# Kernel tuning notes

Measured on AMD Instinct MI355X. Metric: run time of the kernel, lower is better.

Reference implementation:

```python
import jax, jax.numpy as jnp
import numpy as np

B, N_KERNELS, IN_DIM, UNITS = 512, 128, 1024, 1024

def setup_inputs() -> dict:
    key = jax.random.key(0)
    k1, k2 = jax.random.split(key)
    x = jax.random.normal(k1, (B, N_KERNELS, IN_DIM), dtype=jnp.float32)
    kernels = jax.random.normal(k2, (N_KERNELS, IN_DIM, UNITS), dtype=jnp.float32) * 0.02
    return {"x": x, "kernels": kernels}

def reference(x, kernels):
    # Original loops over n_kernels doing x[:, i:i+1, :] @ kernels[i] then softplus.
    # Note: the original's K.bias_add return value is discarded, so bias never
    # affects the output; the faithful math has no bias term.
    # Batched GEMM over the position axis k: [B,K,I] x [K,I,O] -> [B,K,O]
    out = jax.nn.softplus(jnp.einsum('bki,kio->bko', x, kernels))
    return out
```

## Files before the change

kernel.cpp:

```cpp
#include <hip/hip_runtime.h>

#define NKER  128
#define INDIM 1024
#define UNITS 1024

typedef __attribute__((ext_vector_type(8)))  short          bf16x8;
typedef __attribute__((ext_vector_type(4)))  float          f32x4;
typedef __attribute__((ext_vector_type(4)))  unsigned short u16x4;
typedef __attribute__((ext_vector_type(8)))  unsigned short u16x8;

#define LGKM0   asm volatile("s_waitcnt lgkmcnt(0)" ::: "memory")
#define BAR()   __builtin_amdgcn_s_barrier()
#define SCHED0  __builtin_amdgcn_sched_barrier(0)

__device__ __forceinline__ unsigned short f2bf(float f) {
    return __builtin_bit_cast(unsigned short, static_cast<__bf16>(f));
}

__device__ __forceinline__ int swzidx(int r, int k) {
    return r * 32 + ((((k >> 3) ^ ((r >> 1) & 3)) << 3) | (k & 7));
}

struct Stage {
    f32x4 av[4];
    float bv[8];
};

__global__ void __launch_bounds__(512, 2)
dense_local(const float* __restrict__ X, const float* __restrict__ Kn,
            float* __restrict__ Out)
{
    __shared__ __align__(16) unsigned short lA[2][256 * 32];
    __shared__ __align__(16) unsigned short lB[2][128 * 32];

    const int bid  = blockIdx.x;
    const int wg   = (bid & 7) * 256 + (bid >> 3);
    const int kidx = wg >> 4;
    const int tile = wg & 15;
    const int mt   = tile >> 3;
    const int nt   = tile & 7;

    const int t   = threadIdx.x;
    const int l   = t & 63;
    const int w   = t >> 6;
    const int wm  = w >> 1;
    const int wn  = w & 1;
    const int l15 = l & 15, g = l >> 4;

    const size_t MROW = (size_t)NKER * INDIM;

    const float* Abase = X   + (size_t)mt * 256 * MROW + (size_t)kidx * INDIM;
    const float* Bbase = Kn  + (size_t)kidx * INDIM * UNITS + nt * 128;
    float*       Cbase = Out + (size_t)mt * 256 * MROW + (size_t)kidx * UNITS + nt * 128;

    const int ar0 = t >> 3;
    const int ak4 = (t & 7) << 2;
    const int bn  = t & 127;
    const int bkh = t >> 7;

    const float* aTh = Abase + (size_t)ar0 * MROW + ak4;
    const float* bTh = Bbase + (size_t)bkh * 8 * UNITS + bn;
    const float* aP0 = aTh;                const float* bP0 = bTh;
    const float* aP1 = aTh + 32;           const float* bP1 = bTh + (size_t)32 * UNITS;

    f32x4 acc[4][4];
#pragma unroll
    for (int mi = 0; mi < 4; ++mi)
#pragma unroll
        for (int ni = 0; ni < 4; ++ni)
            acc[mi][ni] = f32x4{0.f, 0.f, 0.f, 0.f};

    Stage S0, S1;

    auto loadg = [&](Stage& S, const float*& aP, const float*& bP) {
#pragma unroll
        for (int p = 0; p < 4; ++p)
            S.av[p] = *(const f32x4*)(aP + (size_t)p * 64 * MROW);
#pragma unroll
        for (int j = 0; j < 8; ++j)
            S.bv[j] = bP[(size_t)j * UNITS];
        aP += 64;
        bP += (size_t)64 * UNITS;
    };

    auto writes = [&](const Stage& S, int bb) {
#pragma unroll
        for (int p = 0; p < 4; ++p) {
            u16x4 h;
#pragma unroll
            for (int c = 0; c < 4; ++c) h[c] = f2bf(S.av[p][c]);
            *(u16x4*)&lA[bb][swzidx(ar0 + p * 64, ak4)] = h;
        }
        u16x8 h0;
#pragma unroll
        for (int j = 0; j < 8; ++j) h0[j] = f2bf(S.bv[j]);
        *(u16x8*)&lB[bb][swzidx(bn, bkh * 8)] = h0;
    };

    auto compute = [&](int bb) {
        bf16x8 af[4], bfr[4];
#pragma unroll
        for (int mi = 0; mi < 4; ++mi)
            af[mi] = *(const bf16x8*)&lA[bb][swzidx(wm * 64 + mi * 16 + l15, g * 8)];
#pragma unroll
        for (int ni = 0; ni < 4; ++ni)
            bfr[ni] = *(const bf16x8*)&lB[bb][swzidx(wn * 64 + ni * 16 + l15, g * 8)];
        LGKM0;
        SCHED0;
        __builtin_amdgcn_s_setprio(1);
#pragma unroll
        for (int mi = 0; mi < 4; ++mi)
#pragma unroll
            for (int ni = 0; ni < 4; ++ni)
                acc[mi][ni] = __builtin_amdgcn_mfma_f32_16x16x32_bf16(
                    af[mi], bfr[ni], acc[mi][ni], 0, 0, 0);
        __builtin_amdgcn_s_setprio(0);
    };

    loadg(S0, aP0, bP0);
    loadg(S1, aP1, bP1);
    writes(S0, 0);
    LGKM0;
    BAR();

#pragma unroll 1
    for (int it = 0; it < 15; ++it) {
        loadg(S0, aP0, bP0);
        compute(0);
        BAR();
        writes(S1, 1);
        LGKM0;
        BAR();
        loadg(S1, aP1, bP1);
        compute(1);
        BAR();
        writes(S0, 0);
        LGKM0;
        BAR();
    }

    compute(0);
    BAR();
    writes(S1, 1);
    LGKM0;
    BAR();
    compute(1);

#pragma unroll
    for (int mi = 0; mi < 4; ++mi) {
#pragma unroll
        for (int ni = 0; ni < 4; ++ni) {
            const int n = wn * 64 + ni * 16 + l15;
#pragma unroll
            for (int r = 0; r < 4; ++r) {
                const int m = wm * 64 + mi * 16 + g * 4 + r;
                const float v  = acc[mi][ni][r];
                const float sp = fmaxf(v, 0.0f) + log1pf(__expf(-fabsf(v)));
                Cbase[(size_t)m * MROW + n] = sp;
            }
        }
    }
}

extern "C" void kernel_launch(void* const* d_in, const int* in_sizes, int n_in,
                              void* d_out, int out_size, void* d_ws, size_t ws_size,
                              hipStream_t stream) {
    const float* X  = (const float*)d_in[0];
    const float* Kn = (const float*)d_in[1];
    float* O = (float*)d_out;
    dense_local<<<2048, 512, 0, stream>>>(X, Kn, O);
}
```

Before: 453.1 us.

## Load A fragments directly into registers, dropping the LDS staging for A

A tile rows are now read from global memory straight into the MFMA operand layout, converted to bf16 in registers, and never pass through shared memory. Waves are re-split so each wave owns 32 rows and all 128 columns (2x8 MFMA tiles), which removes the A shared-memory writes and reads and halves LDS use. In exchange each wave re-reads the full B tile from LDS, and the A global loads become less coalesced: each lane reads 32 bytes with a stride of a full row.

```diff
diff --git a/kernel.cpp b/kernel.cpp
--- a/kernel.cpp
+++ b/kernel.cpp
@@ -6,7 +6,6 @@
 
 typedef __attribute__((ext_vector_type(8)))  short          bf16x8;
 typedef __attribute__((ext_vector_type(4)))  float          f32x4;
-typedef __attribute__((ext_vector_type(4)))  unsigned short u16x4;
 typedef __attribute__((ext_vector_type(8)))  unsigned short u16x8;
 
 #define LGKM0   asm volatile("s_waitcnt lgkmcnt(0)" ::: "memory")
@@ -21,16 +20,10 @@
     return r * 32 + ((((k >> 3) ^ ((r >> 1) & 3)) << 3) | (k & 7));
 }
 
-struct Stage {
-    f32x4 av[4];
-    float bv[8];
-};
-
 __global__ void __launch_bounds__(512, 2)
 dense_local(const float* __restrict__ X, const float* __restrict__ Kn,
             float* __restrict__ Out)
 {
-    __shared__ __align__(16) unsigned short lA[2][256 * 32];
     __shared__ __align__(16) unsigned short lB[2][128 * 32];
 
     const int bid  = blockIdx.x;
@@ -43,8 +36,6 @@
     const int t   = threadIdx.x;
     const int l   = t & 63;
     const int w   = t >> 6;
-    const int wm  = w >> 1;
-    const int wn  = w & 1;
     const int l15 = l & 15, g = l >> 4;
 
     const size_t MROW = (size_t)NKER * INDIM;
@@ -53,107 +44,115 @@
     const float* Bbase = Kn  + (size_t)kidx * INDIM * UNITS + nt * 128;
     float*       Cbase = Out + (size_t)mt * 256 * MROW + (size_t)kidx * UNITS + nt * 128;
 
-    const int ar0 = t >> 3;
-    const int ak4 = (t & 7) << 2;
-    const int bn  = t & 127;
-    const int bkh = t >> 7;
+    const float* aP = Abase + (size_t)(w * 32 + l15) * MROW + g * 8;
+    const int bn = t & 127, bkh = t >> 7;
+    const float* bP0 = Bbase + (size_t)bkh * 8 * UNITS + bn;
+    const float* bP1 = bP0 + (size_t)32 * UNITS;
 
-    const float* aTh = Abase + (size_t)ar0 * MROW + ak4;
-    const float* bTh = Bbase + (size_t)bkh * 8 * UNITS + bn;
-    const float* aP0 = aTh;                const float* bP0 = bTh;
-    const float* aP1 = aTh + 32;           const float* bP1 = bTh + (size_t)32 * UNITS;
-
-    f32x4 acc[4][4];
+    f32x4 acc[2][8];
 #pragma unroll
-    for (int mi = 0; mi < 4; ++mi)
+    for (int mi = 0; mi < 2; ++mi)
 #pragma unroll
-        for (int ni = 0; ni < 4; ++ni)
+        for (int ni = 0; ni < 8; ++ni)
             acc[mi][ni] = f32x4{0.f, 0.f, 0.f, 0.f};
 
-    Stage S0, S1;
+    f32x4 aw[2][2];
+    float s0[8], s1[8];
 
-    auto loadg = [&](Stage& S, const float*& aP, const float*& bP) {
+    auto loadA = [&]() {
 #pragma unroll
-        for (int p = 0; p < 4; ++p)
-            S.av[p] = *(const f32x4*)(aP + (size_t)p * 64 * MROW);
+        for (int mi = 0; mi < 2; ++mi) {
+            const float* p = aP + (size_t)mi * 16 * MROW;
+            aw[mi][0] = *(const f32x4*)(p);
+            aw[mi][1] = *(const f32x4*)(p + 4);
+        }
+        aP += 32;
+    };
+    auto loadB = [&](float* S, const float*& bP) {
 #pragma unroll
         for (int j = 0; j < 8; ++j)
-            S.bv[j] = bP[(size_t)j * UNITS];
-        aP += 64;
+            S[j] = bP[(size_t)j * UNITS];
         bP += (size_t)64 * UNITS;
     };
-
-    auto writes = [&](const Stage& S, int bb) {
+    auto writeB = [&](const float* S, int bb) {
+        u16x8 h;
 #pragma unroll
-        for (int p = 0; p < 4; ++p) {
-            u16x4 h;
-#pragma unroll
-            for (int c = 0; c < 4; ++c) h[c] = f2bf(S.av[p][c]);
-            *(u16x4*)&lA[bb][swzidx(ar0 + p * 64, ak4)] = h;
-        }
-        u16x8 h0;
-#pragma unroll
-        for (int j = 0; j < 8; ++j) h0[j] = f2bf(S.bv[j]);
-        *(u16x8*)&lB[bb][swzidx(bn, bkh * 8)] = h0;
+        for (int j = 0; j < 8; ++j) h[j] = f2bf(S[j]);
+        *(u16x8*)&lB[bb][swzidx(bn, bkh * 8)] = h;
     };
 
-    auto compute = [&](int bb) {
-        bf16x8 af[4], bfr[4];
+    bf16x8 af[2];
+    auto cvtA = [&]() {
 #pragma unroll
-        for (int mi = 0; mi < 4; ++mi)
-            af[mi] = *(const bf16x8*)&lA[bb][swzidx(wm * 64 + mi * 16 + l15, g * 8)];
+        for (int mi = 0; mi < 2; ++mi) {
+            u16x8 h;
 #pragma unroll
-        for (int ni = 0; ni < 4; ++ni)
-            bfr[ni] = *(const bf16x8*)&lB[bb][swzidx(wn * 64 + ni * 16 + l15, g * 8)];
+            for (int c = 0; c < 4; ++c) {
+                h[c]     = f2bf(aw[mi][0][c]);
+                h[c + 4] = f2bf(aw[mi][1][c]);
+            }
+            af[mi] = __builtin_bit_cast(bf16x8, h);
+        }
+    };
+
+    bf16x8 bfr[8];
+    auto readB = [&](int bb) {
+#pragma unroll
+        for (int ni = 0; ni < 8; ++ni)
+            bfr[ni] = *(const bf16x8*)&lB[bb][swzidx(ni * 16 + l15, g * 8)];
+    };
+    auto domfma = [&]() {
         LGKM0;
         SCHED0;
         __builtin_amdgcn_s_setprio(1);
 #pragma unroll
-        for (int mi = 0; mi < 4; ++mi)
+        for (int mi = 0; mi < 2; ++mi)
 #pragma unroll
-            for (int ni = 0; ni < 4; ++ni)
+            for (int ni = 0; ni < 8; ++ni)
                 acc[mi][ni] = __builtin_amdgcn_mfma_f32_16x16x32_bf16(
                     af[mi], bfr[ni], acc[mi][ni], 0, 0, 0);
         __builtin_amdgcn_s_setprio(0);
     };
 
-    loadg(S0, aP0, bP0);
-    loadg(S1, aP1, bP1);
-    writes(S0, 0);
+    loadB(s0, bP0);
+    loadB(s1, bP1);
+    loadA();
+    writeB(s0, 0);
     LGKM0;
     BAR();
 
 #pragma unroll 1
-    for (int it = 0; it < 15; ++it) {
-        loadg(S0, aP0, bP0);
-        compute(0);
+    for (int it = 0; it < 16; ++it) {
+        cvtA();
+        loadA();
+        readB(0);
+        if (it < 15) loadB(s0, bP0);
+        domfma();
         BAR();
-        writes(S1, 1);
+        writeB(s1, 1);
         LGKM0;
         BAR();
-        loadg(S1, aP1, bP1);
-        compute(1);
-        BAR();
-        writes(S0, 0);
-        LGKM0;
-        BAR();
+        cvtA();
+        if (it < 15) loadA();
+        readB(1);
+        if (it < 15) loadB(s1, bP1);
+        domfma();
+        if (it < 15) {
+            BAR();
+            writeB(s0, 0);
+            LGKM0;
+            BAR();
+        }
     }
 
-    compute(0);
-    BAR();
-    writes(S1, 1);
-    LGKM0;
-    BAR();
-    compute(1);
-
 #pragma unroll
-    for (int mi = 0; mi < 4; ++mi) {
+    for (int mi = 0; mi < 2; ++mi) {
 #pragma unroll
-        for (int ni = 0; ni < 4; ++ni) {
-            const int n = wn * 64 + ni * 16 + l15;
+        for (int ni = 0; ni < 8; ++ni) {
+            const int n = ni * 16 + l15;
 #pragma unroll
             for (int r = 0; r < 4; ++r) {
-                const int m = wm * 64 + mi * 16 + g * 4 + r;
+                const int m = w * 32 + mi * 16 + g * 4 + r;
                 const float v  = acc[mi][ni][r];
                 const float sp = fmaxf(v, 0.0f) + log1pf(__expf(-fabsf(v)));
                 Cbase[(size_t)m * MROW + n] = sp;
```

After: 561.7 us. 24.0% more time.

## Restructure K-loop into 64-wide tiles split into two interleaved half-phases

Applied to the files above, without the earlier changes.

Each iteration now covers a 64-wide K chunk held as two 32-wide LDS sub-buffers, double-buffered across iterations. The A and B global loads, bf16 conversion and LDS writes for the next chunk are spread across the two MFMA half-phases of the current chunk. The aim is to overlap global memory latency and LDS writes with matrix compute and to reduce the barrier stalls per K step. In exchange, LDS use doubles, more staging registers are live, and there are four barriers per 64-K step, which may hurt occupancy at 2 blocks per CU.

```diff
diff --git a/kernel.cpp b/kernel.cpp
--- a/kernel.cpp
+++ b/kernel.cpp
@@ -21,17 +21,12 @@
     return r * 32 + ((((k >> 3) ^ ((r >> 1) & 3)) << 3) | (k & 7));
 }
 
-struct Stage {
-    f32x4 av[4];
-    float bv[8];
-};
-
 __global__ void __launch_bounds__(512, 2)
 dense_local(const float* __restrict__ X, const float* __restrict__ Kn,
             float* __restrict__ Out)
 {
-    __shared__ __align__(16) unsigned short lA[2][256 * 32];
-    __shared__ __align__(16) unsigned short lB[2][128 * 32];
+    __shared__ __align__(16) unsigned short lA[2][2][256 * 32];
+    __shared__ __align__(16) unsigned short lB[2][2][128 * 32];
 
     const int bid  = blockIdx.x;
     const int wg   = (bid & 7) * 256 + (bid >> 3);
@@ -58,10 +53,8 @@
     const int bn  = t & 127;
     const int bkh = t >> 7;
 
-    const float* aTh = Abase + (size_t)ar0 * MROW + ak4;
-    const float* bTh = Bbase + (size_t)bkh * 8 * UNITS + bn;
-    const float* aP0 = aTh;                const float* bP0 = bTh;
-    const float* aP1 = aTh + 32;           const float* bP1 = bTh + (size_t)32 * UNITS;
+    const float* aP = Abase + (size_t)ar0 * MROW + ak4;
+    const float* bP = Bbase + (size_t)bkh * 8 * UNITS + bn;
 
     f32x4 acc[4][4];
 #pragma unroll
@@ -70,81 +63,103 @@
         for (int ni = 0; ni < 4; ++ni)
             acc[mi][ni] = f32x4{0.f, 0.f, 0.f, 0.f};
 
-    Stage S0, S1;
+    f32x4 SA[4][2];
+    float SB[2][8];
 
-    auto loadg = [&](Stage& S, const float*& aP, const float*& bP) {
+    auto issueA = [&]() {
 #pragma unroll
         for (int p = 0; p < 4; ++p)
-            S.av[p] = *(const f32x4*)(aP + (size_t)p * 64 * MROW);
 #pragma unroll
-        for (int j = 0; j < 8; ++j)
-            S.bv[j] = bP[(size_t)j * UNITS];
+            for (int s = 0; s < 2; ++s)
+                SA[p][s] = *(const f32x4*)(aP + (size_t)p * 64 * MROW + s * 32);
         aP += 64;
+    };
+    auto issueB = [&]() {
+#pragma unroll
+        for (int s = 0; s < 2; ++s)
+#pragma unroll
+            for (int j = 0; j < 8; ++j)
+                SB[s][j] = bP[(size_t)(s * 32 + j) * UNITS];
         bP += (size_t)64 * UNITS;
     };
-
-    auto writes = [&](const Stage& S, int bb) {
+    auto cvtWriteA = [&](int nb) {
 #pragma unroll
-        for (int p = 0; p < 4; ++p) {
-            u16x4 h;
+        for (int p = 0; p < 4; ++p)
 #pragma unroll
-            for (int c = 0; c < 4; ++c) h[c] = f2bf(S.av[p][c]);
-            *(u16x4*)&lA[bb][swzidx(ar0 + p * 64, ak4)] = h;
+            for (int s = 0; s < 2; ++s) {
+                u16x4 h;
+#pragma unroll
+                for (int c = 0; c < 4; ++c) h[c] = f2bf(SA[p][s][c]);
+                *(u16x4*)&lA[nb][s][swzidx(ar0 + p * 64, ak4)] = h;
+            }
+    };
+    auto cvtWriteB = [&](int nb) {
+#pragma unroll
+        for (int s = 0; s < 2; ++s) {
+            u16x8 h;
+#pragma unroll
+            for (int j = 0; j < 8; ++j) h[j] = f2bf(SB[s][j]);
+            *(u16x8*)&lB[nb][s][swzidx(bn, bkh * 8)] = h;
         }
-        u16x8 h0;
-#pragma unroll
-        for (int j = 0; j < 8; ++j) h0[j] = f2bf(S.bv[j]);
-        *(u16x8*)&lB[bb][swzidx(bn, bkh * 8)] = h0;
     };
 
-    auto compute = [&](int bb) {
-        bf16x8 af[4], bfr[4];
+    auto body = [&](int tt, bool wr, bool iss) {
+        const int c = tt & 1, nb = c ^ 1;
+        bf16x8 af0[4], bf0[4], af1[4], bf1[4];
 #pragma unroll
         for (int mi = 0; mi < 4; ++mi)
-            af[mi] = *(const bf16x8*)&lA[bb][swzidx(wm * 64 + mi * 16 + l15, g * 8)];
+            af0[mi] = *(const bf16x8*)&lA[c][0][swzidx(wm * 64 + mi * 16 + l15, g * 8)];
 #pragma unroll
         for (int ni = 0; ni < 4; ++ni)
-            bfr[ni] = *(const bf16x8*)&lB[bb][swzidx(wn * 64 + ni * 16 + l15, g * 8)];
-        LGKM0;
-        SCHED0;
+            bf0[ni] = *(const bf16x8*)&lB[c][0][swzidx(wn * 64 + ni * 16 + l15, g * 8)];
+        if (wr)  cvtWriteA(nb);
+        if (iss) issueA();
+        BAR();
+        LGKM0; SCHED0;
         __builtin_amdgcn_s_setprio(1);
 #pragma unroll
         for (int mi = 0; mi < 4; ++mi)
 #pragma unroll
             for (int ni = 0; ni < 4; ++ni)
                 acc[mi][ni] = __builtin_amdgcn_mfma_f32_16x16x32_bf16(
-                    af[mi], bfr[ni], acc[mi][ni], 0, 0, 0);
+                    af0[mi], bf0[ni], acc[mi][ni], 0, 0, 0);
         __builtin_amdgcn_s_setprio(0);
+        BAR();
+#pragma unroll
+        for (int mi = 0; mi < 4; ++mi)
+            af1[mi] = *(const bf16x8*)&lA[c][1][swzidx(wm * 64 + mi * 16 + l15, g * 8)];
+#pragma unroll
+        for (int ni = 0; ni < 4; ++ni)
+            bf1[ni] = *(const bf16x8*)&lB[c][1][swzidx(wn * 64 + ni * 16 + l15, g * 8)];
+        if (wr)  cvtWriteB(nb);
+        if (iss) issueB();
+        BAR();
+        LGKM0; SCHED0;
+        __builtin_amdgcn_s_setprio(1);
+#pragma unroll
+        for (int mi = 0; mi < 4; ++mi)
+#pragma unroll
+            for (int ni = 0; ni < 4; ++ni)
+                acc[mi][ni] = __builtin_amdgcn_mfma_f32_16x16x32_bf16(
+                    af1[mi], bf1[ni], acc[mi][ni], 0, 0, 0);
+        __builtin_amdgcn_s_setprio(0);
+        BAR();
     };
 
-    loadg(S0, aP0, bP0);
-    loadg(S1, aP1, bP1);
-    writes(S0, 0);
+    issueA();
+    issueB();
+    cvtWriteA(0);
+    issueA();
+    cvtWriteB(0);
+    issueB();
     LGKM0;
     BAR();
 
 #pragma unroll 1
-    for (int it = 0; it < 15; ++it) {
-        loadg(S0, aP0, bP0);
-        compute(0);
-        BAR();
-        writes(S1, 1);
-        LGKM0;
-        BAR();
-        loadg(S1, aP1, bP1);
-        compute(1);
-        BAR();
-        writes(S0, 0);
-        LGKM0;
-        BAR();
-    }
-
-    compute(0);
-    BAR();
-    writes(S1, 1);
-    LGKM0;
-    BAR();
-    compute(1);
+    for (int tt = 0; tt < 14; ++tt)
+        body(tt, true, true);
+    body(14, true, false);
+    body(15, false, false);
 
 #pragma unroll
     for (int mi = 0; mi < 4; ++mi) {
```

After: 474.0 us. 1.05x slower.
